# Performance work log

Hardware: AMD Instinct MI355X
Metric: run time of the kernel (lower is better)

Reference implementation:

```python
import jax, jax.numpy as jnp
import numpy as np

G = 8          # num_groups
GIN = 2048 // G   # group_in_features
GOUT = 2048 // G  # group_out_features


def setup_inputs() -> dict:
    key = jax.random.key(0)
    kx, kw, kb = jax.random.split(key, 3)
    x = jax.random.normal(kx, (8192, 2048), dtype=jnp.float32)
    # per-group linear params, torch nn.Linear default init scale ~ U(-1/sqrt(fan_in), ...)
    bound = 1.0 / np.sqrt(GIN)
    W = jax.random.uniform(kw, (G, GIN, GOUT), minval=-bound, maxval=bound, dtype=jnp.float32)
    b = jax.random.uniform(kb, (G, GOUT), minval=-bound, maxval=bound, dtype=jnp.float32)
    # rational activation coeffs, init p=[1,0,0,0], q=[1,0,0] per group
    p = jnp.tile(jnp.array([1.0, 0.0, 0.0, 0.0], dtype=jnp.float32), (G, 1))
    q = jnp.tile(jnp.array([1.0, 0.0, 0.0], dtype=jnp.float32), (G, 1))
    return {"x": x, "W": W, "b": b, "p": p, "q": q}


def _rational(y, p, q):
    # y: [N, G, GOUT]; p: [G, 4]; q: [G, 3] -> broadcast over N and GOUT
    p = p[None, :, :, None]  # [1,G,4,1]
    q = q[None, :, :, None]  # [1,G,3,1]
    y2 = y * y
    y3 = y2 * y
    num = p[:, :, 0] + p[:, :, 1] * y + p[:, :, 2] * y2 + p[:, :, 3] * y3
    den = 1.0 + jnp.abs(q[:, :, 0] * y + q[:, :, 1] * y2 + q[:, :, 2] * y3)
    return num / den


def reference(x, W, b, p, q):
    N = x.shape[0]
    xg = x.reshape(N, G, GIN)                       # chunk along last dim
    y = jnp.einsum('ngi,gio->ngo', xg, W) + b[None]  # grouped GEMM, [N,G,GOUT]
    out = _rational(y, p, q)
    return out.reshape(N, G * GOUT)                 # cat along last dim
```

## Files before the change

kernel.cpp:

```cpp
#include <hip/hip_runtime.h>
#include <hip/hip_bf16.h>

#define G_ 8
#define GIN_ 256
#define GOUT_ 256
#define NROWS_ 8192
#define LDX_ 2048

typedef __attribute__((ext_vector_type(4))) float f32x4;
typedef __attribute__((ext_vector_type(8))) short bf16x8;

__device__ __forceinline__ void lds_barrier() {
    asm volatile("s_waitcnt lgkmcnt(0)\n\ts_barrier" ::: "memory");
}

__global__ __launch_bounds__(256) void wprep_kernel(const float* __restrict__ W,
                                                    __hip_bfloat16* __restrict__ Wt) {
    __shared__ float tile[64][65];
    const int bid = blockIdx.x;
    const int g  = bid >> 4;
    const int kt = (bid >> 2) & 3;
    const int ct = bid & 3;
    const float* Wg = W + g * (GIN_ * GOUT_);
    __hip_bfloat16* Wo = Wt + (size_t)g * (GIN_ * GOUT_);
    const int lane_o = threadIdx.x & 63;
    const int sub    = threadIdx.x >> 6;
#pragma unroll
    for (int r = 0; r < 16; ++r) {
        int i = r * 4 + sub;
        tile[i][lane_o] = Wg[(kt * 64 + i) * GOUT_ + ct * 64 + lane_o];
    }
    __syncthreads();
    const int col = threadIdx.x & 63;
    const int kgb = threadIdx.x >> 6;
#pragma unroll
    for (int h = 0; h < 2; ++h) {
        const int kg    = kgb + h * 4;
        const int kglob = kt * 64 + kg * 8;
        const int c     = kglob >> 5;
        const int quad  = (kglob >> 3) & 3;
        const int colg  = ct * 64 + col;
        const int cb    = colg >> 4;
        const int c16   = colg & 15;
        union { __hip_bfloat16 hh[8]; bf16x8 v; } cv;
#pragma unroll
        for (int j = 0; j < 8; ++j)
            cv.hh[j] = __float2bfloat16(tile[kg * 8 + j][col]);
        *(bf16x8*)(Wo + (size_t)(c * 16 + cb) * 512 + c16 * 32 + quad * 8) = cv.v;
    }
}

__global__ __launch_bounds__(512, 8) void gkan_kernel(const float* __restrict__ x,
                                                      const __hip_bfloat16* __restrict__ Wt,
                                                      const float* __restrict__ bias,
                                                      const float* __restrict__ pc,
                                                      const float* __restrict__ qc,
                                                      float* __restrict__ out) {
    __shared__ __align__(16) __hip_bfloat16 As[8192];

    const int bid  = blockIdx.x;
    const int g    = bid & 7;
    const int row0 = (bid >> 3) * 32;

    const int t    = threadIdx.x;
    const int wave = t >> 6;
    const int lane = t & 63;
    const int lm   = lane & 15;
    const int q    = lane >> 4;

    const int row = t >> 4;
    const int su  = t & 15;
    const float* xs = x + (size_t)(row0 + row) * LDX_ + g * GIN_ + su * 8;
    f32x4 a0 = *(const f32x4*)(xs);
    f32x4 a1 = *(const f32x4*)(xs + 4);
    f32x4 b0 = *(const f32x4*)(xs + 128);
    f32x4 b1 = *(const f32x4*)(xs + 132);

    {
        const int rblk = row >> 4, r16 = row & 15, rx = row & 3;
        const int c0 = su >> 2, quad = su & 3;
        const int slot = (quad ^ rx) * 8 + r16 * 32;
        union { __hip_bfloat16 hh[8]; bf16x8 v; } ca, cb;
        ca.hh[0] = __float2bfloat16(a0.x); ca.hh[1] = __float2bfloat16(a0.y);
        ca.hh[2] = __float2bfloat16(a0.z); ca.hh[3] = __float2bfloat16(a0.w);
        ca.hh[4] = __float2bfloat16(a1.x); ca.hh[5] = __float2bfloat16(a1.y);
        ca.hh[6] = __float2bfloat16(a1.z); ca.hh[7] = __float2bfloat16(a1.w);
        cb.hh[0] = __float2bfloat16(b0.x); cb.hh[1] = __float2bfloat16(b0.y);
        cb.hh[2] = __float2bfloat16(b0.z); cb.hh[3] = __float2bfloat16(b0.w);
        cb.hh[4] = __float2bfloat16(b1.x); cb.hh[5] = __float2bfloat16(b1.y);
        cb.hh[6] = __float2bfloat16(b1.z); cb.hh[7] = __float2bfloat16(b1.w);
        *(bf16x8*)(As + (c0 * 2 + rblk) * 512 + slot)       = ca.v;
        *(bf16x8*)(As + ((4 + c0) * 2 + rblk) * 512 + slot) = cb.v;
    }
    lds_barrier();

    f32x4 acc[2][2] = {};
    const __hip_bfloat16* bp = Wt + (size_t)g * (GIN_ * GOUT_)
                                  + (wave * 2) * 512 + lm * 32 + q * 8;
    const __hip_bfloat16* ap = As + lm * 32 + ((q ^ (lm & 3)) * 8);
#pragma unroll 1
    for (int c = 0; c < 8; ++c) {
        const bf16x8 bf0 = *(const bf16x8*)(bp);
        const bf16x8 bf1 = *(const bf16x8*)(bp + 512);
        const bf16x8 af0 = *(const bf16x8*)(ap);
        const bf16x8 af1 = *(const bf16x8*)(ap + 512);
        acc[0][0] = __builtin_amdgcn_mfma_f32_16x16x32_bf16(af0, bf0, acc[0][0], 0, 0, 0);
        acc[0][1] = __builtin_amdgcn_mfma_f32_16x16x32_bf16(af0, bf1, acc[0][1], 0, 0, 0);
        acc[1][0] = __builtin_amdgcn_mfma_f32_16x16x32_bf16(af1, bf0, acc[1][0], 0, 0, 0);
        acc[1][1] = __builtin_amdgcn_mfma_f32_16x16x32_bf16(af1, bf1, acc[1][1], 0, 0, 0);
        bp += 16 * 512;
        ap += 2 * 512;
    }

    const float p0 = pc[g * 4 + 0], p1 = pc[g * 4 + 1];
    const float p2 = pc[g * 4 + 2], p3 = pc[g * 4 + 3];
    const float q0 = qc[g * 3 + 0], q1 = qc[g * 3 + 1], q2 = qc[g * 3 + 2];
    float bb[2];
#pragma unroll
    for (int nt = 0; nt < 2; ++nt)
        bb[nt] = bias[g * GOUT_ + wave * 32 + nt * 16 + lm];

#pragma unroll
    for (int nt = 0; nt < 2; ++nt) {
        const int col = g * GOUT_ + wave * 32 + nt * 16 + lm;
#pragma unroll
        for (int mt = 0; mt < 2; ++mt)
#pragma unroll
            for (int r = 0; r < 4; ++r) {
                const int row_o = row0 + mt * 16 + q * 4 + r;
                const float y   = acc[mt][nt][r] + bb[nt];
                const float num = p0 + y * (p1 + y * (p2 + y * p3));
                const float den = 1.0f + fabsf(y * (q0 + y * (q1 + y * q2)));
                out[(size_t)row_o * LDX_ + col] = num * __builtin_amdgcn_rcpf(den);
            }
    }
}

extern "C" void kernel_launch(void* const* d_in, const int* in_sizes, int n_in,
                              void* d_out, int out_size, void* d_ws, size_t ws_size,
                              hipStream_t stream) {
    const float* x = (const float*)d_in[0];
    const float* W = (const float*)d_in[1];
    const float* b = (const float*)d_in[2];
    const float* p = (const float*)d_in[3];
    const float* q = (const float*)d_in[4];
    float* out = (float*)d_out;

    __hip_bfloat16* Wt = (__hip_bfloat16*)d_ws;

    wprep_kernel<<<128, 256, 0, stream>>>(W, Wt);
    gkan_kernel<<<2048, 512, 0, stream>>>(x, Wt, b, p, q, out);
}
```

Measured before the change: 133.3 us.

## Drop LDS staging; load A fragments directly from global with register prefetch

Each wave now reads its x fragment directly from global memory, converting it to bf16 in registers instead of staging through shared memory behind a barrier. Blocks shrink to 16 rows by 128 columns with 4 waves, and the grid grows to 8192 blocks. The next K-chunk of x and W is prefetched into registers while the current MFMAs run. This removes LDS traffic and barrier stalls, but x is read redundantly by multiple waves and blocks, relying on cache to absorb the extra traffic.

```diff
diff --git a/kernel.cpp b/kernel.cpp
--- a/kernel.cpp
+++ b/kernel.cpp
@@ -9,10 +9,6 @@
 
 typedef __attribute__((ext_vector_type(4))) float f32x4;
 typedef __attribute__((ext_vector_type(8))) short bf16x8;
-
-__device__ __forceinline__ void lds_barrier() {
-    asm volatile("s_waitcnt lgkmcnt(0)\n\ts_barrier" ::: "memory");
-}
 
 __global__ __launch_bounds__(256) void wprep_kernel(const float* __restrict__ W,
                                                     __hip_bfloat16* __restrict__ Wt) {
@@ -50,89 +46,77 @@
     }
 }
 
-__global__ __launch_bounds__(512, 8) void gkan_kernel(const float* __restrict__ x,
+__device__ __forceinline__ bf16x8 cvt8(const f32x4 a, const f32x4 b) {
+    union { __hip_bfloat16 h[8]; bf16x8 v; } u;
+    u.h[0] = __float2bfloat16(a.x); u.h[1] = __float2bfloat16(a.y);
+    u.h[2] = __float2bfloat16(a.z); u.h[3] = __float2bfloat16(a.w);
+    u.h[4] = __float2bfloat16(b.x); u.h[5] = __float2bfloat16(b.y);
+    u.h[6] = __float2bfloat16(b.z); u.h[7] = __float2bfloat16(b.w);
+    return u.v;
+}
+
+__global__ __launch_bounds__(256, 8) void gkan_kernel(const float* __restrict__ x,
                                                       const __hip_bfloat16* __restrict__ Wt,
                                                       const float* __restrict__ bias,
                                                       const float* __restrict__ pc,
                                                       const float* __restrict__ qc,
                                                       float* __restrict__ out) {
-    __shared__ __align__(16) __hip_bfloat16 As[8192];
-
     const int bid  = blockIdx.x;
     const int g    = bid & 7;
-    const int row0 = (bid >> 3) * 32;
+    const int ch   = (bid >> 3) & 1;
+    const int row0 = (bid >> 4) * 16;
 
     const int t    = threadIdx.x;
     const int wave = t >> 6;
     const int lane = t & 63;
     const int lm   = lane & 15;
     const int q    = lane >> 4;
+    const int colbase = ch * 128 + wave * 32;
 
-    const int row = t >> 4;
-    const int su  = t & 15;
-    const float* xs = x + (size_t)(row0 + row) * LDX_ + g * GIN_ + su * 8;
-    f32x4 a0 = *(const f32x4*)(xs);
-    f32x4 a1 = *(const f32x4*)(xs + 4);
-    f32x4 b0 = *(const f32x4*)(xs + 128);
-    f32x4 b1 = *(const f32x4*)(xs + 132);
+    const float* ap = x + (size_t)(row0 + lm) * LDX_ + g * GIN_ + q * 8;
+    const __hip_bfloat16* bp = Wt + (size_t)g * (GIN_ * GOUT_)
+                                  + (size_t)(ch * 8 + wave * 2) * 512
+                                  + lm * 32 + q * 8;
 
-    {
-        const int rblk = row >> 4, r16 = row & 15, rx = row & 3;
-        const int c0 = su >> 2, quad = su & 3;
-        const int slot = (quad ^ rx) * 8 + r16 * 32;
-        union { __hip_bfloat16 hh[8]; bf16x8 v; } ca, cb;
-        ca.hh[0] = __float2bfloat16(a0.x); ca.hh[1] = __float2bfloat16(a0.y);
-        ca.hh[2] = __float2bfloat16(a0.z); ca.hh[3] = __float2bfloat16(a0.w);
-        ca.hh[4] = __float2bfloat16(a1.x); ca.hh[5] = __float2bfloat16(a1.y);
-        ca.hh[6] = __float2bfloat16(a1.z); ca.hh[7] = __float2bfloat16(a1.w);
-        cb.hh[0] = __float2bfloat16(b0.x); cb.hh[1] = __float2bfloat16(b0.y);
-        cb.hh[2] = __float2bfloat16(b0.z); cb.hh[3] = __float2bfloat16(b0.w);
-        cb.hh[4] = __float2bfloat16(b1.x); cb.hh[5] = __float2bfloat16(b1.y);
-        cb.hh[6] = __float2bfloat16(b1.z); cb.hh[7] = __float2bfloat16(b1.w);
-        *(bf16x8*)(As + (c0 * 2 + rblk) * 512 + slot)       = ca.v;
-        *(bf16x8*)(As + ((4 + c0) * 2 + rblk) * 512 + slot) = cb.v;
-    }
-    lds_barrier();
+    f32x4 ar0 = *(const f32x4*)(ap);
+    f32x4 ar1 = *(const f32x4*)(ap + 4);
+    bf16x8 cb0 = *(const bf16x8*)(bp);
+    bf16x8 cb1 = *(const bf16x8*)(bp + 512);
 
-    f32x4 acc[2][2] = {};
-    const __hip_bfloat16* bp = Wt + (size_t)g * (GIN_ * GOUT_)
-                                  + (wave * 2) * 512 + lm * 32 + q * 8;
-    const __hip_bfloat16* ap = As + lm * 32 + ((q ^ (lm & 3)) * 8);
-#pragma unroll 1
+    f32x4 acc[2] = {};
+#pragma unroll
     for (int c = 0; c < 8; ++c) {
-        const bf16x8 bf0 = *(const bf16x8*)(bp);
-        const bf16x8 bf1 = *(const bf16x8*)(bp + 512);
-        const bf16x8 af0 = *(const bf16x8*)(ap);
-        const bf16x8 af1 = *(const bf16x8*)(ap + 512);
-        acc[0][0] = __builtin_amdgcn_mfma_f32_16x16x32_bf16(af0, bf0, acc[0][0], 0, 0, 0);
-        acc[0][1] = __builtin_amdgcn_mfma_f32_16x16x32_bf16(af0, bf1, acc[0][1], 0, 0, 0);
-        acc[1][0] = __builtin_amdgcn_mfma_f32_16x16x32_bf16(af1, bf0, acc[1][0], 0, 0, 0);
-        acc[1][1] = __builtin_amdgcn_mfma_f32_16x16x32_bf16(af1, bf1, acc[1][1], 0, 0, 0);
-        bp += 16 * 512;
-        ap += 2 * 512;
+        f32x4 nr0, nr1; bf16x8 nb0, nb1;
+        if (c < 7) {
+            const float* an = ap + (c + 1) * 32;
+            nr0 = *(const f32x4*)(an);
+            nr1 = *(const f32x4*)(an + 4);
+            const __hip_bfloat16* bn = bp + (size_t)(c + 1) * (16 * 512);
+            nb0 = *(const bf16x8*)(bn);
+            nb1 = *(const bf16x8*)(bn + 512);
+        }
+        const bf16x8 af = cvt8(ar0, ar1);
+        acc[0] = __builtin_amdgcn_mfma_f32_16x16x32_bf16(af, cb0, acc[0], 0, 0, 0);
+        acc[1] = __builtin_amdgcn_mfma_f32_16x16x32_bf16(af, cb1, acc[1], 0, 0, 0);
+        if (c < 7) { ar0 = nr0; ar1 = nr1; cb0 = nb0; cb1 = nb1; }
     }
 
     const float p0 = pc[g * 4 + 0], p1 = pc[g * 4 + 1];
     const float p2 = pc[g * 4 + 2], p3 = pc[g * 4 + 3];
     const float q0 = qc[g * 3 + 0], q1 = qc[g * 3 + 1], q2 = qc[g * 3 + 2];
-    float bb[2];
-#pragma unroll
-    for (int nt = 0; nt < 2; ++nt)
-        bb[nt] = bias[g * GOUT_ + wave * 32 + nt * 16 + lm];
 
 #pragma unroll
     for (int nt = 0; nt < 2; ++nt) {
-        const int col = g * GOUT_ + wave * 32 + nt * 16 + lm;
+        const int col = g * GOUT_ + colbase + nt * 16 + lm;
+        const float bb = bias[g * GOUT_ + colbase + nt * 16 + lm];
 #pragma unroll
-        for (int mt = 0; mt < 2; ++mt)
-#pragma unroll
-            for (int r = 0; r < 4; ++r) {
-                const int row_o = row0 + mt * 16 + q * 4 + r;
-                const float y   = acc[mt][nt][r] + bb[nt];
-                const float num = p0 + y * (p1 + y * (p2 + y * p3));
-                const float den = 1.0f + fabsf(y * (q0 + y * (q1 + y * q2)));
-                out[(size_t)row_o * LDX_ + col] = num * __builtin_amdgcn_rcpf(den);
-            }
+        for (int r = 0; r < 4; ++r) {
+            const int row_o = row0 + q * 4 + r;
+            const float y   = acc[nt][r] + bb;
+            const float num = p0 + y * (p1 + y * (p2 + y * p3));
+            const float den = 1.0f + fabsf(y * (q0 + y * (q1 + y * q2)));
+            out[(size_t)row_o * LDX_ + col] = num * __builtin_amdgcn_rcpf(den);
+        }
     }
 }
 
@@ -149,5 +133,5 @@
     __hip_bfloat16* Wt = (__hip_bfloat16*)d_ws;
 
     wprep_kernel<<<128, 256, 0, stream>>>(W, Wt);
-    gkan_kernel<<<2048, 512, 0, stream>>>(x, Wt, b, p, q, out);
+    gkan_kernel<<<8192, 256, 0, stream>>>(x, Wt, b, p, q, out);
 }
```

Result: slower. 191.6 us (+43.8%).

## Load x tile directly into LDS as fp32 and convert to bf16 at fragment read

Applied to the files above, without the earlier changes.

The x tile is now staged with global_load_lds straight into shared memory as fp32, using an XOR-swizzled layout, instead of going through registers and being converted to bf16 before the LDS store. Each wave converts to bf16 when it reads its MFMA A fragments. This removes the register round trip and the up-front conversion. In exchange LDS use doubles to 32 KB per block, which may lower occupancy, and each wave repeats the conversion work on the reads.

```diff
diff --git a/kernel.cpp b/kernel.cpp
--- a/kernel.cpp
+++ b/kernel.cpp
@@ -9,10 +9,6 @@
 
 typedef __attribute__((ext_vector_type(4))) float f32x4;
 typedef __attribute__((ext_vector_type(8))) short bf16x8;
-
-__device__ __forceinline__ void lds_barrier() {
-    asm volatile("s_waitcnt lgkmcnt(0)\n\ts_barrier" ::: "memory");
-}
 
 __global__ __launch_bounds__(256) void wprep_kernel(const float* __restrict__ W,
                                                     __hip_bfloat16* __restrict__ Wt) {
@@ -50,13 +46,22 @@
     }
 }
 
+__device__ __forceinline__ bf16x8 cvt8(const f32x4 a, const f32x4 b) {
+    union { __hip_bfloat16 h[8]; bf16x8 v; } u;
+    u.h[0] = __float2bfloat16(a.x); u.h[1] = __float2bfloat16(a.y);
+    u.h[2] = __float2bfloat16(a.z); u.h[3] = __float2bfloat16(a.w);
+    u.h[4] = __float2bfloat16(b.x); u.h[5] = __float2bfloat16(b.y);
+    u.h[6] = __float2bfloat16(b.z); u.h[7] = __float2bfloat16(b.w);
+    return u.v;
+}
+
 __global__ __launch_bounds__(512, 8) void gkan_kernel(const float* __restrict__ x,
                                                       const __hip_bfloat16* __restrict__ Wt,
                                                       const float* __restrict__ bias,
                                                       const float* __restrict__ pc,
                                                       const float* __restrict__ qc,
                                                       float* __restrict__ out) {
-    __shared__ __align__(16) __hip_bfloat16 As[8192];
+    __shared__ __align__(16) float As[32 * 256];
 
     const int bid  = blockIdx.x;
     const int g    = bid & 7;
@@ -68,48 +73,43 @@
     const int lm   = lane & 15;
     const int q    = lane >> 4;
 
-    const int row = t >> 4;
-    const int su  = t & 15;
-    const float* xs = x + (size_t)(row0 + row) * LDX_ + g * GIN_ + su * 8;
-    f32x4 a0 = *(const f32x4*)(xs);
-    f32x4 a1 = *(const f32x4*)(xs + 4);
-    f32x4 b0 = *(const f32x4*)(xs + 128);
-    f32x4 b1 = *(const f32x4*)(xs + 132);
+    {
+        const float* xrow = x + (size_t)row0 * LDX_ + g * GIN_;
+#pragma unroll
+        for (int r = 0; r < 4; ++r) {
+            const int row  = r * 8 + wave;
+            const int gidx = lane ^ wave;
+            const float* src = xrow + (size_t)row * LDX_ + gidx * 4;
+            __builtin_amdgcn_global_load_lds(
+                (const __attribute__((address_space(1))) void*)src,
+                (__attribute__((address_space(3))) void*)((char*)As + r * 8192 + t * 16),
+                16, 0, 0);
+        }
+    }
 
-    {
-        const int rblk = row >> 4, r16 = row & 15, rx = row & 3;
-        const int c0 = su >> 2, quad = su & 3;
-        const int slot = (quad ^ rx) * 8 + r16 * 32;
-        union { __hip_bfloat16 hh[8]; bf16x8 v; } ca, cb;
-        ca.hh[0] = __float2bfloat16(a0.x); ca.hh[1] = __float2bfloat16(a0.y);
-        ca.hh[2] = __float2bfloat16(a0.z); ca.hh[3] = __float2bfloat16(a0.w);
-        ca.hh[4] = __float2bfloat16(a1.x); ca.hh[5] = __float2bfloat16(a1.y);
-        ca.hh[6] = __float2bfloat16(a1.z); ca.hh[7] = __float2bfloat16(a1.w);
-        cb.hh[0] = __float2bfloat16(b0.x); cb.hh[1] = __float2bfloat16(b0.y);
-        cb.hh[2] = __float2bfloat16(b0.z); cb.hh[3] = __float2bfloat16(b0.w);
-        cb.hh[4] = __float2bfloat16(b1.x); cb.hh[5] = __float2bfloat16(b1.y);
-        cb.hh[6] = __float2bfloat16(b1.z); cb.hh[7] = __float2bfloat16(b1.w);
-        *(bf16x8*)(As + (c0 * 2 + rblk) * 512 + slot)       = ca.v;
-        *(bf16x8*)(As + ((4 + c0) * 2 + rblk) * 512 + slot) = cb.v;
-    }
-    lds_barrier();
+    asm volatile("s_waitcnt vmcnt(0) lgkmcnt(0)\n\ts_barrier" ::: "memory");
 
     f32x4 acc[2][2] = {};
     const __hip_bfloat16* bp = Wt + (size_t)g * (GIN_ * GOUT_)
                                   + (wave * 2) * 512 + lm * 32 + q * 8;
-    const __hip_bfloat16* ap = As + lm * 32 + ((q ^ (lm & 3)) * 8);
 #pragma unroll 1
     for (int c = 0; c < 8; ++c) {
         const bf16x8 bf0 = *(const bf16x8*)(bp);
         const bf16x8 bf1 = *(const bf16x8*)(bp + 512);
-        const bf16x8 af0 = *(const bf16x8*)(ap);
-        const bf16x8 af1 = *(const bf16x8*)(ap + 512);
-        acc[0][0] = __builtin_amdgcn_mfma_f32_16x16x32_bf16(af0, bf0, acc[0][0], 0, 0, 0);
-        acc[0][1] = __builtin_amdgcn_mfma_f32_16x16x32_bf16(af0, bf1, acc[0][1], 0, 0, 0);
-        acc[1][0] = __builtin_amdgcn_mfma_f32_16x16x32_bf16(af1, bf0, acc[1][0], 0, 0, 0);
-        acc[1][1] = __builtin_amdgcn_mfma_f32_16x16x32_bf16(af1, bf1, acc[1][1], 0, 0, 0);
+        const int s0 = c * 8 + q * 2;
+        bf16x8 af[2];
+#pragma unroll
+        for (int mt = 0; mt < 2; ++mt) {
+            const int rr = mt * 16 + lm;
+            const f32x4 lo = *(const f32x4*)(As + rr * 256 + ((s0 ^ (lm & 7)) * 4));
+            const f32x4 hi = *(const f32x4*)(As + rr * 256 + (((s0 + 1) ^ (lm & 7)) * 4));
+            af[mt] = cvt8(lo, hi);
+        }
+        acc[0][0] = __builtin_amdgcn_mfma_f32_16x16x32_bf16(af[0], bf0, acc[0][0], 0, 0, 0);
+        acc[0][1] = __builtin_amdgcn_mfma_f32_16x16x32_bf16(af[0], bf1, acc[0][1], 0, 0, 0);
+        acc[1][0] = __builtin_amdgcn_mfma_f32_16x16x32_bf16(af[1], bf0, acc[1][0], 0, 0, 0);
+        acc[1][1] = __builtin_amdgcn_mfma_f32_16x16x32_bf16(af[1], bf1, acc[1][1], 0, 0, 0);
         bp += 16 * 512;
-        ap += 2 * 512;
     }
 
     const float p0 = pc[g * 4 + 0], p1 = pc[g * 4 + 1];
```

New measurement: 135.3 us. Within noise of the previous version (+1.5%).
